# Kernel optimization log

Measured on AMD Instinct MI355X. Metric: run time of the kernel, lower is better.

Reference implementation:

```python
import jax, jax.numpy as jnp
import numpy as np

B, D, T, H = 256, 256, 512, 512  # batch, input_dim, seq_len, hidden_dim


def setup_inputs() -> dict:
    key = jax.random.key(0)
    ks = jax.random.split(key, 7)
    s = 1.0 / np.sqrt(H)
    u = lambda k, shape: jax.random.uniform(k, shape, jnp.float32, -s, s)
    return {
        "x": jax.random.normal(ks[0], (B, D, T), jnp.float32),
        "W_ih": u(ks[1], (4 * H, D)),   # gate order: i, f, g, o (PyTorch)
        "W_hh": u(ks[2], (4 * H, H)),
        "b_ih": u(ks[3], (4 * H,)),
        "b_hh": u(ks[4], (4 * H,)),
        "W_mlp": u(ks[5], (1, H)),      # Linear(hidden_dim, num_classes=1)
        "b_mlp": u(ks[6], (1,)),
    }


def reference(x, W_ih, W_hh, b_ih, b_hh, W_mlp, b_mlp):
    # x: (B, D, T) -> (T, B, D), matching the two transposes in LSTM_model
    xs = jnp.transpose(x, (2, 0, 1))
    # Precompute input contributions for all timesteps: (T, B, 4H)
    x_gates = jnp.einsum('tbd,gd->tbg', xs, W_ih) + b_ih + b_hh
    Hh = W_hh.shape[1]

    def step(carry, xg):
        h, c = carry
        g = xg + h @ W_hh.T                      # (B, 4H)
        i = jax.nn.sigmoid(g[:, 0 * Hh:1 * Hh])
        f = jax.nn.sigmoid(g[:, 1 * Hh:2 * Hh])
        gg = jnp.tanh(g[:, 2 * Hh:3 * Hh])
        o = jax.nn.sigmoid(g[:, 3 * Hh:4 * Hh])
        c_new = f * c + i * gg
        h_new = o * jnp.tanh(c_new)
        return (h_new, c_new), h_new

    h0 = jnp.zeros((x.shape[0], Hh), x.dtype)
    c0 = jnp.zeros((x.shape[0], Hh), x.dtype)
    _, h_t = jax.lax.scan(step, (h0, c0), x_gates)   # (T, B, H)

    # MLP with num_layers=1: single Linear(H, 1) then sigmoid, per timestep.
    logits = jnp.einsum('tbh,h->tb', h_t, W_mlp[0]) + b_mlp[0]  # (T, B)
    out = jax.nn.sigmoid(logits)
    return out.T  # (B, T), matching out[..., t] layout
```

## Files before the change

### kernel.cpp

```cpp
#include <hip/hip_runtime.h>
#include <stdint.h>

#define BSZ 256
#define DIN 256
#define TLEN 512
#define HDIM 512
#define POISON 0xAAAAAAAAu

typedef _Float16 h16;
typedef unsigned int u32;
typedef unsigned long long u64;
typedef __attribute__((ext_vector_type(8))) _Float16 half8;
typedef __attribute__((ext_vector_type(4))) float f32x4;

__device__ __forceinline__ float fast_sigmoid(float x) {
    return 1.0f / (1.0f + __expf(-x));
}
__device__ __forceinline__ float fast_tanh(float x) {
    return 2.0f / (1.0f + __expf(-2.0f * x)) - 1.0f;
}

__device__ __forceinline__ u64 load_agent_u64(const u64* p) {
    return __hip_atomic_load((u64*)p, __ATOMIC_RELAXED, __HIP_MEMORY_SCOPE_AGENT);
}
__device__ __forceinline__ void store_agent_u32(u32* p, u32 v) {
    __hip_atomic_store(p, v, __ATOMIC_RELAXED, __HIP_MEMORY_SCOPE_AGENT);
}

__global__ __launch_bounds__(256)
void transpose_x(const float* __restrict__ x, h16* __restrict__ xT) {
    __shared__ h16 tl[64][72];
    const int tid = threadIdx.x;
    const int tb  = blockIdx.x & 7;
    const int bd0 = (blockIdx.x >> 3) * 64;
    const int t0  = tb * 64;
#pragma unroll
    for (int p = 0; p < 4; ++p) {
        int idx  = p * 256 + tid;
        int bd_l = idx >> 4;
        int t4   = idx & 15;
        float4 v = *(const float4*)(x + (size_t)(bd0 + bd_l) * TLEN + t0 + t4 * 4);
        tl[t4 * 4 + 0][bd_l] = (h16)v.x;
        tl[t4 * 4 + 1][bd_l] = (h16)v.y;
        tl[t4 * 4 + 2][bd_l] = (h16)v.z;
        tl[t4 * 4 + 3][bd_l] = (h16)v.w;
    }
    __syncthreads();
#pragma unroll
    for (int p = 0; p < 2; ++p) {
        int idx = p * 256 + tid;
        int t_l = idx >> 3;
        int seg = idx & 7;
        uint4 v = *(const uint4*)&tl[t_l][seg * 8];
        *(uint4*)(xT + (size_t)(t0 + t_l) * (BSZ * DIN) + bd0 + seg * 8) = v;
    }
}

__global__ __launch_bounds__(256, 1)
void lstm_kernel(const float* __restrict__ x,
                 const float* __restrict__ W_ih,
                 const float* __restrict__ W_hh,
                 const float* __restrict__ b_ih,
                 const float* __restrict__ b_hh,
                 const float* __restrict__ W_mlp,
                 const h16* __restrict__ xT,
                 int use_xT,
                 h16* __restrict__ hslots,
                 float* __restrict__ logits,
                 float* __restrict__ part,
                 int use_part)
{
    __shared__ h16  h_sw[16][64][8];
    __shared__ h16  x_sw[8][8][64][8];
    __shared__ float g_lds[16][132];

    const int tid  = threadIdx.x;
    const int bid  = blockIdx.x;
    const int clique = bid & 15;
    const int mem    = bid >> 4;
    const int lane = tid & 63;
    const int w    = tid >> 6;
    const int l15  = lane & 15;
    const int lq   = lane >> 4;
    const int cb   = clique * 16;

    half8 whh[2][16], wih[2][8];
#pragma unroll
    for (int i = 0; i < 2; ++i) {
        const int nrow = w * HDIM + mem * 32 + i * 16 + l15;
        const float* wr = W_hh + (size_t)nrow * HDIM;
#pragma unroll
        for (int kk = 0; kk < 16; ++kk) {
            const float* p = wr + kk * 32 + lq * 8;
            half8 v;
#pragma unroll
            for (int j = 0; j < 8; ++j) v[j] = (h16)p[j];
            whh[i][kk] = v;
        }
        const float* wr2 = W_ih + (size_t)nrow * DIN;
#pragma unroll
        for (int kk = 0; kk < 8; ++kk) {
            const float* p = wr2 + kk * 32 + lq * 8;
            half8 v;
#pragma unroll
            for (int j = 0; j < 8; ++j) v[j] = (h16)p[j];
            wih[i][kk] = v;
        }
    }

    const int eb = tid >> 4;
    const int ej = tid & 15;
    const int jg = mem * 32 + ej * 2;
    float bias[8];
#pragma unroll
    for (int q = 0; q < 4; ++q) {
        bias[q * 2 + 0] = b_ih[q * HDIM + jg]     + b_hh[q * HDIM + jg];
        bias[q * 2 + 1] = b_ih[q * HDIM + jg + 1] + b_hh[q * HDIM + jg + 1];
    }
    const float wm0 = W_mlp[jg], wm1 = W_mlp[jg + 1];
    float c0 = 0.0f, c1 = 0.0f;
    float pbuf[8];

    u32  qoff[8];
    h16* hdst4[4];
#pragma unroll
    for (int it = 0; it < 4; ++it) {
        int c   = it * 256 + tid;
        int L   = c & 63;
        int kk  = c >> 6;
        int b   = L & 15;
        int k0  = kk * 32 + (L >> 4) * 8;
        qoff[it * 2 + 0] = (u32)((b * HDIM + k0) >> 2);
        qoff[it * 2 + 1] = qoff[it * 2 + 0] + 1;
        hdst4[it] = &h_sw[kk][L][0];
    }
    const size_t own_off = (size_t)(cb + eb) * HDIM + jg;

    for (int t = 0; t < TLEN; ++t) {
        if (use_xT) {
#pragma unroll
            for (int it = 0; it < 2; ++it) {
                int c  = it * 256 + tid;
                int L  = c & 63;
                int kk = c >> 6;
                int b  = L & 15;
                int d0 = kk * 32 + (L >> 4) * 8;
                uint4 v = *(const uint4*)(xT + (size_t)t * (BSZ * DIN)
                                             + (size_t)(cb + b) * DIN + d0);
                *(uint4*)&x_sw[0][kk][L][0] = v;
            }
        } else if ((t & 7) == 0) {
            const int d   = tid;
            const int kk  = d >> 5;
            const int dlq = (d >> 3) & 3;
            const int j   = d & 7;
#pragma unroll 4
            for (int b = 0; b < 16; ++b) {
                const float* p = x + ((size_t)(cb + b) * DIN + d) * TLEN + t;
                float4 v0 = *(const float4*)p;
                float4 v1 = *(const float4*)(p + 4);
                int L = b | (dlq << 4);
                x_sw[0][kk][L][j] = (h16)v0.x;
                x_sw[1][kk][L][j] = (h16)v0.y;
                x_sw[2][kk][L][j] = (h16)v0.z;
                x_sw[3][kk][L][j] = (h16)v0.w;
                x_sw[4][kk][L][j] = (h16)v1.x;
                x_sw[5][kk][L][j] = (h16)v1.y;
                x_sw[6][kk][L][j] = (h16)v1.z;
                x_sw[7][kk][L][j] = (h16)v1.w;
            }
        }
        const int sb = use_xT ? 0 : (t & 7);

        if (t > 0) {
            asm volatile("s_waitcnt vmcnt(0)" ::: "memory");
            store_agent_u32((u32*)(hslots + (size_t)((t + 3) & 7) * BSZ * HDIM
                                          + own_off), POISON);

            const u64* hb = (const u64*)(hslots + ((size_t)(t & 7) * BSZ + cb) * HDIM);
            u64 q[8];
            u32 pend = 0xFFu;
            while (pend) {
#pragma unroll
                for (int i = 0; i < 8; ++i)
                    if (pend & (1u << i)) q[i] = load_agent_u64(hb + qoff[i]);
                u32 np = 0;
#pragma unroll
                for (int i = 0; i < 8; ++i)
                    if (pend & (1u << i)) {
                        u32 lo = (u32)q[i], hi = (u32)(q[i] >> 32);
                        if (lo == POISON || hi == POISON) np |= 1u << i;
                    }
                pend = np;
                if (pend) __builtin_amdgcn_s_sleep(1);
            }
#pragma unroll
            for (int it = 0; it < 4; ++it) {
                union { u64 qq[2]; uint4 v; } pk;
                pk.qq[0] = q[it * 2 + 0];
                pk.qq[1] = q[it * 2 + 1];
                *(uint4*)hdst4[it] = pk.v;
            }
        }
        __syncthreads();

        f32x4 acc0 = {0.f, 0.f, 0.f, 0.f};
        f32x4 acc1 = {0.f, 0.f, 0.f, 0.f};
#pragma unroll
        for (int kk = 0; kk < 8; ++kk) {
            half8 a = *(const half8*)&x_sw[sb][kk][lane][0];
            acc0 = __builtin_amdgcn_mfma_f32_16x16x32_f16(a, wih[0][kk], acc0, 0, 0, 0);
            acc1 = __builtin_amdgcn_mfma_f32_16x16x32_f16(a, wih[1][kk], acc1, 0, 0, 0);
        }
        if (t > 0) {
#pragma unroll
            for (int kk = 0; kk < 16; ++kk) {
                half8 a = *(const half8*)&h_sw[kk][lane][0];
                acc0 = __builtin_amdgcn_mfma_f32_16x16x32_f16(a, whh[0][kk], acc0, 0, 0, 0);
                acc1 = __builtin_amdgcn_mfma_f32_16x16x32_f16(a, whh[1][kk], acc1, 0, 0, 0);
            }
        }
        {
            const int col0 = w * 32 + l15;
            const int col1 = w * 32 + 16 + l15;
#pragma unroll
            for (int r = 0; r < 4; ++r) {
                g_lds[lq * 4 + r][col0] = acc0[r];
                g_lds[lq * 4 + r][col1] = acc1[r];
            }
        }
        __syncthreads();

        float mlp_p;
        {
            float gi0 = g_lds[eb][ej * 2]          + bias[0];
            float gi1 = g_lds[eb][ej * 2 + 1]      + bias[1];
            float gf0 = g_lds[eb][32 + ej * 2]     + bias[2];
            float gf1 = g_lds[eb][32 + ej * 2 + 1] + bias[3];
            float gg0 = g_lds[eb][64 + ej * 2]     + bias[4];
            float gg1 = g_lds[eb][64 + ej * 2 + 1] + bias[5];
            float go0 = g_lds[eb][96 + ej * 2]     + bias[6];
            float go1 = g_lds[eb][96 + ej * 2 + 1] + bias[7];
            c0 = fast_sigmoid(gf0) * c0 + fast_sigmoid(gi0) * fast_tanh(gg0);
            c1 = fast_sigmoid(gf1) * c1 + fast_sigmoid(gi1) * fast_tanh(gg1);
            float h0 = fast_sigmoid(go0) * fast_tanh(c0);
            float h1 = fast_sigmoid(go1) * fast_tanh(c1);

            union { h16 h2[2]; u32 uu; } pk;
            pk.h2[0] = (h16)h0; pk.h2[1] = (h16)h1;
            if (pk.uu == POISON) pk.uu ^= 1u;
            store_agent_u32((u32*)(hslots + (size_t)((t + 1) & 7) * BSZ * HDIM
                                          + own_off), pk.uu);

            float p = h0 * wm0 + h1 * wm1;
            p += __shfl_xor(p, 1);
            p += __shfl_xor(p, 2);
            p += __shfl_xor(p, 4);
            p += __shfl_xor(p, 8);
            mlp_p = p;
            pbuf[t & 7] = p;
            if (use_part && (t & 7) == 7 && ej == 0) {
                float* pd = &part[((size_t)mem * BSZ + cb + eb) * TLEN + (t - 7)];
                float4 v0, v1;
                v0.x = pbuf[0]; v0.y = pbuf[1]; v0.z = pbuf[2]; v0.w = pbuf[3];
                v1.x = pbuf[4]; v1.y = pbuf[5]; v1.z = pbuf[6]; v1.w = pbuf[7];
                *(float4*)pd       = v0;
                *(float4*)(pd + 4) = v1;
            }
        }
        if (!use_part && ej == 0) {
            atomicAdd(&logits[(size_t)(cb + eb) * TLEN + t], mlp_p);
        }
    }
}

__global__ __launch_bounds__(256)
void final_sigmoid(const float* __restrict__ logits,
                   const float* __restrict__ part,
                   int use_part,
                   const float* __restrict__ b_mlp,
                   float* __restrict__ out) {
    int i = blockIdx.x * 256 + threadIdx.x;
    float v;
    if (use_part) {
        int t = i & (TLEN - 1);
        int b = i >> 9;
        v = 0.f;
#pragma unroll
        for (int mm = 0; mm < 16; ++mm)
            v += part[((size_t)mm * BSZ + b) * TLEN + t];
    } else {
        v = logits[i];
    }
    v += b_mlp[0];
    out[i] = 1.0f / (1.0f + __expf(-v));
}

extern "C" void kernel_launch(void* const* d_in, const int* in_sizes, int n_in,
                              void* d_out, int out_size, void* d_ws, size_t ws_size,
                              hipStream_t stream) {
    const float* x     = (const float*)d_in[0];
    const float* W_ih  = (const float*)d_in[1];
    const float* W_hh  = (const float*)d_in[2];
    const float* b_ih  = (const float*)d_in[3];
    const float* b_hh  = (const float*)d_in[4];
    const float* W_mlp = (const float*)d_in[5];
    const float* b_mlp = (const float*)d_in[6];
    float* out = (float*)d_out;

    char* ws = (char*)d_ws;
    float* logits = (float*)ws;
    h16*   hslots = (h16*)(ws + 1048576);
    float* part   = (float*)(ws + 4194304);
    h16*   xT     = (h16*)(ws + 20971520);
    const int use_part = (ws_size >= (size_t)20971520) ? 1 : 0;
    const int use_xT   = (ws_size >= (size_t)88080384) ? 1 : 0;

    hipMemsetAsync(d_ws, 0, 524288, stream);

    if (use_xT) {
        transpose_x<<<8192, 256, 0, stream>>>(x, xT);
    }
    lstm_kernel<<<256, 256, 0, stream>>>(x, W_ih, W_hh, b_ih, b_hh, W_mlp,
                                         xT, use_xT, hslots, logits,
                                         part, use_part);
    final_sigmoid<<<(BSZ * TLEN) / 256, 256, 0, stream>>>(logits, part, use_part,
                                                          b_mlp, out);
}
```

Before: 2.103 ms.

## Overlap x-gate MFMAs and next-step x prefetch with hidden-state polling

The transposed-x path now double-buffers x in LDS: the next timestep's tile is loaded into registers early and written to the alternate buffer after the gate MFMAs. The input-projection MFMAs run before the spin-wait on the other blocks' hidden state, and the first h loads are issued before the poison store, so the x work hides part of the cross-block sync latency. The recurrent MFMA chain is split into two independent accumulator pairs that are summed at the end, to shorten the dependent MFMA chain. This adds register pressure and relies on the x_sw buffer having at least two slots.

After: 1.857 ms. 1.13x faster.

```diff
diff --git a/kernel.cpp b/kernel.cpp
--- a/kernel.cpp
+++ b/kernel.cpp
@@ -136,20 +136,22 @@
     }
     const size_t own_off = (size_t)(cb + eb) * HDIM + jg;
 
+    const int pfL = tid & 63;
+    const int pfk = tid >> 6;
+    const int pfb = pfL & 15;
+    const int pfd = pfk * 32 + ((pfL >> 4) * 8);
+    const h16* pf_src = xT + (size_t)(cb + pfb) * DIN + pfd;
+
+    if (use_xT) {
+        uint4 v0 = *(const uint4*)(pf_src);
+        uint4 v1 = *(const uint4*)(pf_src + 128);
+        *(uint4*)&x_sw[0][pfk][pfL][0]     = v0;
+        *(uint4*)&x_sw[0][pfk + 4][pfL][0] = v1;
+    }
+    __syncthreads();
+
     for (int t = 0; t < TLEN; ++t) {
-        if (use_xT) {
-#pragma unroll
-            for (int it = 0; it < 2; ++it) {
-                int c  = it * 256 + tid;
-                int L  = c & 63;
-                int kk = c >> 6;
-                int b  = L & 15;
-                int d0 = kk * 32 + (L >> 4) * 8;
-                uint4 v = *(const uint4*)(xT + (size_t)t * (BSZ * DIN)
-                                             + (size_t)(cb + b) * DIN + d0);
-                *(uint4*)&x_sw[0][kk][L][0] = v;
-            }
-        } else if ((t & 7) == 0) {
+        if (!use_xT && (t & 7) == 0) {
             const int d   = tid;
             const int kk  = d >> 5;
             const int dlq = (d >> 3) & 3;
@@ -170,20 +172,53 @@
                 x_sw[7][kk][L][j] = (h16)v1.w;
             }
         }
-        const int sb = use_xT ? 0 : (t & 7);
-
+
+        u64 q[8];
+        u32 pend = 0;
+        const u64* hb = nullptr;
         if (t > 0) {
+            hb = (const u64*)(hslots + ((size_t)(t & 7) * BSZ + cb) * HDIM);
+#pragma unroll
+            for (int i = 0; i < 8; ++i) q[i] = load_agent_u64(hb + qoff[i]);
             asm volatile("s_waitcnt vmcnt(0)" ::: "memory");
             store_agent_u32((u32*)(hslots + (size_t)((t + 3) & 7) * BSZ * HDIM
                                           + own_off), POISON);
-
-            const u64* hb = (const u64*)(hslots + ((size_t)(t & 7) * BSZ + cb) * HDIM);
-            u64 q[8];
-            u32 pend = 0xFFu;
-            while (pend) {
+            u32 np = 0;
+#pragma unroll
+            for (int i = 0; i < 8; ++i) {
+                u32 lo = (u32)q[i], hi = (u32)(q[i] >> 32);
+                if (lo == POISON || hi == POISON) np |= 1u << i;
+            }
+            pend = np;
+            if (pend) {
 #pragma unroll
                 for (int i = 0; i < 8; ++i)
                     if (pend & (1u << i)) q[i] = load_agent_u64(hb + qoff[i]);
+            }
+        }
+
+        uint4 pf0, pf1;
+        const int havepf = (use_xT && (t + 1) < TLEN);
+        if (havepf) {
+            const h16* ps = pf_src + (size_t)(t + 1) * (BSZ * DIN);
+            pf0 = *(const uint4*)ps;
+            pf1 = *(const uint4*)(ps + 128);
+        }
+
+        f32x4 acc0 = {0.f, 0.f, 0.f, 0.f};
+        f32x4 acc1 = {0.f, 0.f, 0.f, 0.f};
+        if (use_xT) {
+            const int sx = t & 1;
+#pragma unroll
+            for (int kk = 0; kk < 8; ++kk) {
+                half8 a = *(const half8*)&x_sw[sx][kk][lane][0];
+                acc0 = __builtin_amdgcn_mfma_f32_16x16x32_f16(a, wih[0][kk], acc0, 0, 0, 0);
+                acc1 = __builtin_amdgcn_mfma_f32_16x16x32_f16(a, wih[1][kk], acc1, 0, 0, 0);
+            }
+        }
+
+        if (t > 0) {
+            while (pend) {
                 u32 np = 0;
 #pragma unroll
                 for (int i = 0; i < 8; ++i)
@@ -192,7 +227,12 @@
                         if (lo == POISON || hi == POISON) np |= 1u << i;
                     }
                 pend = np;
-                if (pend) __builtin_amdgcn_s_sleep(1);
+                if (pend) {
+                    __builtin_amdgcn_s_sleep(1);
+#pragma unroll
+                    for (int i = 0; i < 8; ++i)
+                        if (pend & (1u << i)) q[i] = load_agent_u64(hb + qoff[i]);
+                }
             }
 #pragma unroll
             for (int it = 0; it < 4; ++it) {
@@ -204,20 +244,26 @@
         }
         __syncthreads();
 
-        f32x4 acc0 = {0.f, 0.f, 0.f, 0.f};
-        f32x4 acc1 = {0.f, 0.f, 0.f, 0.f};
-#pragma unroll
-        for (int kk = 0; kk < 8; ++kk) {
-            half8 a = *(const half8*)&x_sw[sb][kk][lane][0];
-            acc0 = __builtin_amdgcn_mfma_f32_16x16x32_f16(a, wih[0][kk], acc0, 0, 0, 0);
-            acc1 = __builtin_amdgcn_mfma_f32_16x16x32_f16(a, wih[1][kk], acc1, 0, 0, 0);
-        }
+        if (!use_xT) {
+            const int sb = t & 7;
+#pragma unroll
+            for (int kk = 0; kk < 8; ++kk) {
+                half8 a = *(const half8*)&x_sw[sb][kk][lane][0];
+                acc0 = __builtin_amdgcn_mfma_f32_16x16x32_f16(a, wih[0][kk], acc0, 0, 0, 0);
+                acc1 = __builtin_amdgcn_mfma_f32_16x16x32_f16(a, wih[1][kk], acc1, 0, 0, 0);
+            }
+        }
+        f32x4 acc0b = {0.f, 0.f, 0.f, 0.f};
+        f32x4 acc1b = {0.f, 0.f, 0.f, 0.f};
         if (t > 0) {
 #pragma unroll
-            for (int kk = 0; kk < 16; ++kk) {
+            for (int kk = 0; kk < 8; ++kk) {
                 half8 a = *(const half8*)&h_sw[kk][lane][0];
-                acc0 = __builtin_amdgcn_mfma_f32_16x16x32_f16(a, whh[0][kk], acc0, 0, 0, 0);
-                acc1 = __builtin_amdgcn_mfma_f32_16x16x32_f16(a, whh[1][kk], acc1, 0, 0, 0);
+                half8 b = *(const half8*)&h_sw[kk + 8][lane][0];
+                acc0  = __builtin_amdgcn_mfma_f32_16x16x32_f16(a, whh[0][kk],     acc0,  0, 0, 0);
+                acc1  = __builtin_amdgcn_mfma_f32_16x16x32_f16(a, whh[1][kk],     acc1,  0, 0, 0);
+                acc0b = __builtin_amdgcn_mfma_f32_16x16x32_f16(b, whh[0][kk + 8], acc0b, 0, 0, 0);
+                acc1b = __builtin_amdgcn_mfma_f32_16x16x32_f16(b, whh[1][kk + 8], acc1b, 0, 0, 0);
             }
         }
         {
@@ -225,9 +271,14 @@
             const int col1 = w * 32 + 16 + l15;
 #pragma unroll
             for (int r = 0; r < 4; ++r) {
-                g_lds[lq * 4 + r][col0] = acc0[r];
-                g_lds[lq * 4 + r][col1] = acc1[r];
-            }
+                g_lds[lq * 4 + r][col0] = acc0[r] + acc0b[r];
+                g_lds[lq * 4 + r][col1] = acc1[r] + acc1b[r];
+            }
+        }
+        if (havepf) {
+            const int sx1 = (t + 1) & 1;
+            *(uint4*)&x_sw[sx1][pfk][pfL][0]     = pf0;
+            *(uint4*)&x_sw[sx1][pfk + 4][pfL][0] = pf1;
         }
         __syncthreads();
 
```

## Remove LDS staging and block barriers; make each wave own its gate units

Applied to the files above, without the earlier changes.

Weight rows are remapped so each wave holds all four gates for its own 8 hidden units. The gate combine can then go through a per-wave LDS slice with no __syncthreads. Hidden-state and x operands are loaded straight from global memory into MFMA registers instead of being staged through shared memory, and the x tile for the next step is prefetched. The h polling is issued before the x-projection MFMAs so it overlaps them, and the recurrent MFMA chain is split into two accumulators. MLP partials are stored as fp16 in 64 slices, which adds rounding error and more reduction work in the final kernel, and each lane now issues more global loads.

Result: slower. 7.564 ms (+259.6%).

```diff
diff --git a/kernel.cpp b/kernel.cpp
--- a/kernel.cpp
+++ b/kernel.cpp
@@ -67,12 +67,10 @@
                  int use_xT,
                  h16* __restrict__ hslots,
                  float* __restrict__ logits,
-                 float* __restrict__ part,
+                 h16* __restrict__ part2,
                  int use_part)
 {
-    __shared__ h16  h_sw[16][64][8];
-    __shared__ h16  x_sw[8][8][64][8];
-    __shared__ float g_lds[16][132];
+    __shared__ float gw[4][16][36];
 
     const int tid  = threadIdx.x;
     const int bid  = blockIdx.x;
@@ -87,7 +85,9 @@
     half8 whh[2][16], wih[2][8];
 #pragma unroll
     for (int i = 0; i < 2; ++i) {
-        const int nrow = w * HDIM + mem * 32 + i * 16 + l15;
+        const int gate = i * 2 + (l15 >> 3);
+        const int unit = mem * 32 + w * 8 + (l15 & 7);
+        const int nrow = gate * HDIM + unit;
         const float* wr = W_hh + (size_t)nrow * HDIM;
 #pragma unroll
         for (int kk = 0; kk < 16; ++kk) {
@@ -108,9 +108,7 @@
         }
     }
 
-    const int eb = tid >> 4;
-    const int ej = tid & 15;
-    const int jg = mem * 32 + ej * 2;
+    const int jg = mem * 32 + w * 8 + 2 * lq;
     float bias[8];
 #pragma unroll
     for (int q = 0; q < 4; ++q) {
@@ -121,126 +119,142 @@
     float c0 = 0.0f, c1 = 0.0f;
     float pbuf[8];
 
-    u32  qoff[8];
-    h16* hdst4[4];
-#pragma unroll
-    for (int it = 0; it < 4; ++it) {
-        int c   = it * 256 + tid;
-        int L   = c & 63;
-        int kk  = c >> 6;
-        int b   = L & 15;
-        int k0  = kk * 32 + (L >> 4) * 8;
-        qoff[it * 2 + 0] = (u32)((b * HDIM + k0) >> 2);
-        qoff[it * 2 + 1] = qoff[it * 2 + 0] + 1;
-        hdst4[it] = &h_sw[kk][L][0];
-    }
-    const size_t own_off = (size_t)(cb + eb) * HDIM + jg;
+    const u32 base_u64 = (u32)(((cb + l15) * HDIM + lq * 8) >> 2);
+    const u64* hsl = (const u64*)hslots;
+    const u32 slot_u64 = (BSZ * HDIM) >> 2;
+
+    const size_t own_off = (size_t)(cb + l15) * HDIM + jg;
+
+    const h16* xb = xT + (size_t)(cb + l15) * DIN + lq * 8;
+
+    uint4 xf[8];
+    if (use_xT) {
+#pragma unroll
+        for (int kk = 0; kk < 8; ++kk)
+            xf[kk] = *(const uint4*)(xb + kk * 32);
+    }
 
     for (int t = 0; t < TLEN; ++t) {
-        if (use_xT) {
-#pragma unroll
-            for (int it = 0; it < 2; ++it) {
-                int c  = it * 256 + tid;
-                int L  = c & 63;
-                int kk = c >> 6;
-                int b  = L & 15;
-                int d0 = kk * 32 + (L >> 4) * 8;
-                uint4 v = *(const uint4*)(xT + (size_t)t * (BSZ * DIN)
-                                             + (size_t)(cb + b) * DIN + d0);
-                *(uint4*)&x_sw[0][kk][L][0] = v;
-            }
-        } else if ((t & 7) == 0) {
-            const int d   = tid;
-            const int kk  = d >> 5;
-            const int dlq = (d >> 3) & 3;
-            const int j   = d & 7;
-#pragma unroll 4
-            for (int b = 0; b < 16; ++b) {
-                const float* p = x + ((size_t)(cb + b) * DIN + d) * TLEN + t;
-                float4 v0 = *(const float4*)p;
-                float4 v1 = *(const float4*)(p + 4);
-                int L = b | (dlq << 4);
-                x_sw[0][kk][L][j] = (h16)v0.x;
-                x_sw[1][kk][L][j] = (h16)v0.y;
-                x_sw[2][kk][L][j] = (h16)v0.z;
-                x_sw[3][kk][L][j] = (h16)v0.w;
-                x_sw[4][kk][L][j] = (h16)v1.x;
-                x_sw[5][kk][L][j] = (h16)v1.y;
-                x_sw[6][kk][L][j] = (h16)v1.z;
-                x_sw[7][kk][L][j] = (h16)v1.w;
-            }
-        }
-        const int sb = use_xT ? 0 : (t & 7);
-
+        u64 q[32];
+        u32 pend = 0;
+        const u64* hb = nullptr;
         if (t > 0) {
+            hb = hsl + (size_t)(t & 7) * slot_u64 + base_u64;
+#pragma unroll
+            for (int f = 0; f < 16; ++f) {
+                q[2 * f]     = load_agent_u64(hb + f * 8);
+                q[2 * f + 1] = load_agent_u64(hb + f * 8 + 1);
+            }
             asm volatile("s_waitcnt vmcnt(0)" ::: "memory");
             store_agent_u32((u32*)(hslots + (size_t)((t + 3) & 7) * BSZ * HDIM
                                           + own_off), POISON);
-
-            const u64* hb = (const u64*)(hslots + ((size_t)(t & 7) * BSZ + cb) * HDIM);
-            u64 q[8];
-            u32 pend = 0xFFu;
-            while (pend) {
-#pragma unroll
-                for (int i = 0; i < 8; ++i)
-                    if (pend & (1u << i)) q[i] = load_agent_u64(hb + qoff[i]);
+#pragma unroll
+            for (int f = 0; f < 16; ++f) {
+                u32 a0 = (u32)q[2 * f],     a1 = (u32)(q[2 * f] >> 32);
+                u32 b0 = (u32)q[2 * f + 1], b1 = (u32)(q[2 * f + 1] >> 32);
+                u32 bad = (a0 == POISON) | (a1 == POISON) |
+                          (b0 == POISON) | (b1 == POISON);
+                pend |= bad << f;
+            }
+            if (__any(pend != 0)) {
+#pragma unroll
+                for (int f = 0; f < 16; ++f)
+                    if (pend & (1u << f)) {
+                        q[2 * f]     = load_agent_u64(hb + f * 8);
+                        q[2 * f + 1] = load_agent_u64(hb + f * 8 + 1);
+                    }
+            }
+        }
+
+        f32x4 acc0 = {0.f, 0.f, 0.f, 0.f};
+        f32x4 acc1 = {0.f, 0.f, 0.f, 0.f};
+        if (use_xT) {
+#pragma unroll
+            for (int kk = 0; kk < 8; ++kk) {
+                union { uint4 u; half8 h; } ua;
+                ua.u = xf[kk];
+                acc0 = __builtin_amdgcn_mfma_f32_16x16x32_f16(ua.h, wih[0][kk], acc0, 0, 0, 0);
+                acc1 = __builtin_amdgcn_mfma_f32_16x16x32_f16(ua.h, wih[1][kk], acc1, 0, 0, 0);
+            }
+        } else {
+#pragma unroll
+            for (int kk = 0; kk < 8; ++kk) {
+                half8 a;
+#pragma unroll
+                for (int j = 0; j < 8; ++j)
+                    a[j] = (h16)x[((size_t)(cb + l15) * DIN + kk * 32 + lq * 8 + j) * TLEN + t];
+                acc0 = __builtin_amdgcn_mfma_f32_16x16x32_f16(a, wih[0][kk], acc0, 0, 0, 0);
+                acc1 = __builtin_amdgcn_mfma_f32_16x16x32_f16(a, wih[1][kk], acc1, 0, 0, 0);
+            }
+        }
+
+        if (use_xT && t + 1 < TLEN) {
+            const h16* ps = xb + (size_t)(t + 1) * (BSZ * DIN);
+#pragma unroll
+            for (int kk = 0; kk < 8; ++kk)
+                xf[kk] = *(const uint4*)(ps + kk * 32);
+        }
+
+        if (t > 0) {
+            while (__any(pend != 0)) {
                 u32 np = 0;
 #pragma unroll
-                for (int i = 0; i < 8; ++i)
-                    if (pend & (1u << i)) {
-                        u32 lo = (u32)q[i], hi = (u32)(q[i] >> 32);
-                        if (lo == POISON || hi == POISON) np |= 1u << i;
+                for (int f = 0; f < 16; ++f)
+                    if (pend & (1u << f)) {
+                        u32 a0 = (u32)q[2 * f],     a1 = (u32)(q[2 * f] >> 32);
+                        u32 b0 = (u32)q[2 * f + 1], b1 = (u32)(q[2 * f + 1] >> 32);
+                        u32 bad = (a0 == POISON) | (a1 == POISON) |
+                                  (b0 == POISON) | (b1 == POISON);
+                        np |= bad << f;
                     }
                 pend = np;
-                if (pend) __builtin_amdgcn_s_sleep(1);
-            }
-#pragma unroll
-            for (int it = 0; it < 4; ++it) {
-                union { u64 qq[2]; uint4 v; } pk;
-                pk.qq[0] = q[it * 2 + 0];
-                pk.qq[1] = q[it * 2 + 1];
-                *(uint4*)hdst4[it] = pk.v;
-            }
-        }
-        __syncthreads();
-
-        f32x4 acc0 = {0.f, 0.f, 0.f, 0.f};
-        f32x4 acc1 = {0.f, 0.f, 0.f, 0.f};
-#pragma unroll
-        for (int kk = 0; kk < 8; ++kk) {
-            half8 a = *(const half8*)&x_sw[sb][kk][lane][0];
-            acc0 = __builtin_amdgcn_mfma_f32_16x16x32_f16(a, wih[0][kk], acc0, 0, 0, 0);
-            acc1 = __builtin_amdgcn_mfma_f32_16x16x32_f16(a, wih[1][kk], acc1, 0, 0, 0);
-        }
+                if (__any(pend != 0)) {
+                    __builtin_amdgcn_s_sleep(1);
+#pragma unroll
+                    for (int f = 0; f < 16; ++f)
+                        if (pend & (1u << f)) {
+                            q[2 * f]     = load_agent_u64(hb + f * 8);
+                            q[2 * f + 1] = load_agent_u64(hb + f * 8 + 1);
+                        }
+                }
+            }
+        }
+
+        f32x4 acc0b = {0.f, 0.f, 0.f, 0.f};
+        f32x4 acc1b = {0.f, 0.f, 0.f, 0.f};
         if (t > 0) {
 #pragma unroll
-            for (int kk = 0; kk < 16; ++kk) {
-                half8 a = *(const half8*)&h_sw[kk][lane][0];
-                acc0 = __builtin_amdgcn_mfma_f32_16x16x32_f16(a, whh[0][kk], acc0, 0, 0, 0);
-                acc1 = __builtin_amdgcn_mfma_f32_16x16x32_f16(a, whh[1][kk], acc1, 0, 0, 0);
-            }
-        }
+            for (int f = 0; f < 8; ++f) {
+                union { u64 qq[2]; half8 h; } ua, ub;
+                ua.qq[0] = q[2 * f];
+                ua.qq[1] = q[2 * f + 1];
+                ub.qq[0] = q[2 * (f + 8)];
+                ub.qq[1] = q[2 * (f + 8) + 1];
+                acc0  = __builtin_amdgcn_mfma_f32_16x16x32_f16(ua.h, whh[0][f],     acc0,  0, 0, 0);
+                acc1  = __builtin_amdgcn_mfma_f32_16x16x32_f16(ua.h, whh[1][f],     acc1,  0, 0, 0);
+                acc0b = __builtin_amdgcn_mfma_f32_16x16x32_f16(ub.h, whh[0][f + 8], acc0b, 0, 0, 0);
+                acc1b = __builtin_amdgcn_mfma_f32_16x16x32_f16(ub.h, whh[1][f + 8], acc1b, 0, 0, 0);
+            }
+        }
+
         {
-            const int col0 = w * 32 + l15;
-            const int col1 = w * 32 + 16 + l15;
 #pragma unroll
             for (int r = 0; r < 4; ++r) {
-                g_lds[lq * 4 + r][col0] = acc0[r];
-                g_lds[lq * 4 + r][col1] = acc1[r];
-            }
-        }
-        __syncthreads();
-
-        float mlp_p;
+                gw[w][lq * 4 + r][l15]      = acc0[r] + acc0b[r];
+                gw[w][lq * 4 + r][16 + l15] = acc1[r] + acc1b[r];
+            }
+        }
+        asm volatile("s_waitcnt lgkmcnt(0)" ::: "memory");
+
         {
-            float gi0 = g_lds[eb][ej * 2]          + bias[0];
-            float gi1 = g_lds[eb][ej * 2 + 1]      + bias[1];
-            float gf0 = g_lds[eb][32 + ej * 2]     + bias[2];
-            float gf1 = g_lds[eb][32 + ej * 2 + 1] + bias[3];
-            float gg0 = g_lds[eb][64 + ej * 2]     + bias[4];
-            float gg1 = g_lds[eb][64 + ej * 2 + 1] + bias[5];
-            float go0 = g_lds[eb][96 + ej * 2]     + bias[6];
-            float go1 = g_lds[eb][96 + ej * 2 + 1] + bias[7];
+            float gi0 = gw[w][l15][2 * lq]      + bias[0];
+            float gi1 = gw[w][l15][2 * lq + 1]  + bias[1];
+            float gf0 = gw[w][l15][8 + 2 * lq]  + bias[2];
+            float gf1 = gw[w][l15][8 + 2 * lq + 1] + bias[3];
+            float gg0 = gw[w][l15][16 + 2 * lq] + bias[4];
+            float gg1 = gw[w][l15][16 + 2 * lq + 1] + bias[5];
+            float go0 = gw[w][l15][24 + 2 * lq] + bias[6];
+            float go1 = gw[w][l15][24 + 2 * lq + 1] + bias[7];
             c0 = fast_sigmoid(gf0) * c0 + fast_sigmoid(gi0) * fast_tanh(gg0);
             c1 = fast_sigmoid(gf1) * c1 + fast_sigmoid(gi1) * fast_tanh(gg1);
             float h0 = fast_sigmoid(go0) * fast_tanh(c0);
@@ -253,30 +267,26 @@
                                           + own_off), pk.uu);
 
             float p = h0 * wm0 + h1 * wm1;
-            p += __shfl_xor(p, 1);
-            p += __shfl_xor(p, 2);
-            p += __shfl_xor(p, 4);
-            p += __shfl_xor(p, 8);
-            mlp_p = p;
+            p += __shfl_xor(p, 16);
+            p += __shfl_xor(p, 32);
             pbuf[t & 7] = p;
-            if (use_part && (t & 7) == 7 && ej == 0) {
-                float* pd = &part[((size_t)mem * BSZ + cb + eb) * TLEN + (t - 7)];
-                float4 v0, v1;
-                v0.x = pbuf[0]; v0.y = pbuf[1]; v0.z = pbuf[2]; v0.w = pbuf[3];
-                v1.x = pbuf[4]; v1.y = pbuf[5]; v1.z = pbuf[6]; v1.w = pbuf[7];
-                *(float4*)pd       = v0;
-                *(float4*)(pd + 4) = v1;
-            }
-        }
-        if (!use_part && ej == 0) {
-            atomicAdd(&logits[(size_t)(cb + eb) * TLEN + t], mlp_p);
+            if (use_part && (t & 7) == 7 && lq == 0) {
+                union { h16 hh[8]; uint4 v; } pp;
+#pragma unroll
+                for (int s = 0; s < 8; ++s) pp.hh[s] = (h16)pbuf[s];
+                h16* pd = part2 + ((size_t)(mem * 4 + w) * BSZ + cb + l15) * TLEN + (t - 7);
+                *(uint4*)pd = pp.v;
+            }
+            if (!use_part && lq == 0) {
+                atomicAdd(&logits[(size_t)(cb + l15) * TLEN + t], p);
+            }
         }
     }
 }
 
 __global__ __launch_bounds__(256)
 void final_sigmoid(const float* __restrict__ logits,
-                   const float* __restrict__ part,
+                   const h16* __restrict__ part2,
                    int use_part,
                    const float* __restrict__ b_mlp,
                    float* __restrict__ out) {
@@ -287,8 +297,8 @@
         int b = i >> 9;
         v = 0.f;
 #pragma unroll
-        for (int mm = 0; mm < 16; ++mm)
-            v += part[((size_t)mm * BSZ + b) * TLEN + t];
+        for (int mm = 0; mm < 64; ++mm)
+            v += (float)part2[((size_t)mm * BSZ + b) * TLEN + t];
     } else {
         v = logits[i];
     }
@@ -311,7 +321,7 @@
     char* ws = (char*)d_ws;
     float* logits = (float*)ws;
     h16*   hslots = (h16*)(ws + 1048576);
-    float* part   = (float*)(ws + 4194304);
+    h16*   part2  = (h16*)(ws + 4194304);
     h16*   xT     = (h16*)(ws + 20971520);
     const int use_part = (ws_size >= (size_t)20971520) ? 1 : 0;
     const int use_xT   = (ws_size >= (size_t)88080384) ? 1 : 0;
@@ -323,7 +333,7 @@
     }
     lstm_kernel<<<256, 256, 0, stream>>>(x, W_ih, W_hh, b_ih, b_hh, W_mlp,
                                          xT, use_xT, hslots, logits,
-                                         part, use_part);
-    final_sigmoid<<<(BSZ * TLEN) / 256, 256, 0, stream>>>(logits, part, use_part,
+                                         part2, use_part);
+    final_sigmoid<<<(BSZ * TLEN) / 256, 256, 0, stream>>>(logits, part2, use_part,
                                                           b_mlp, out);
 }
```
